# Kernel optimization log

Hardware: AMD Instinct MI355X
Metric: run time of the kernel (lower is better)

Reference implementation:

```python
import jax, jax.numpy as jnp
import numpy as np

N, NFEAT, NHID, NCLASS, NHEADS = 50000, 512, 256, 64, 8
C1 = NHID // NHEADS  # 32 per-head channels, layer 1
NEG_SLOPE = 0.2


def setup_inputs() -> dict:
    key = jax.random.key(0)
    ks = jax.random.split(key, 10)
    x = jax.random.normal(ks[0], (N, NFEAT), dtype=jnp.float32)
    edge_idx = jax.random.randint(ks[1], (2, 800000), 0, N, dtype=jnp.int64)
    s = 0.05
    return {
        "x": x,
        "edge_idx": edge_idx,
        "W1": jax.random.normal(ks[2], (NFEAT, NHEADS, C1), dtype=jnp.float32) * s,
        "a1_src": jax.random.normal(ks[3], (NHEADS, C1), dtype=jnp.float32) * s,
        "a1_dst": jax.random.normal(ks[4], (NHEADS, C1), dtype=jnp.float32) * s,
        "b1": jnp.zeros((NHID,), dtype=jnp.float32),
        "W2": jax.random.normal(ks[5], (NHID, NHEADS, NCLASS), dtype=jnp.float32) * s,
        "a2_src": jax.random.normal(ks[6], (NHEADS, NCLASS), dtype=jnp.float32) * s,
        "a2_dst": jax.random.normal(ks[7], (NHEADS, NCLASS), dtype=jnp.float32) * s,
        "b2": jnp.zeros((NCLASS,), dtype=jnp.float32),
    }


def gat_conv(x, src, dst, W, a_src, a_dst, b, concat):
    # x: [N, F_in]; W: [F_in, H, C]; a_*: [H, C]; src/dst: [E]
    h = jnp.einsum("nf,fhc->nhc", x, W)             # [N, H, C]
    e_src = jnp.sum(h * a_src, axis=-1)              # [N, H]
    e_dst = jnp.sum(h * a_dst, axis=-1)              # [N, H]
    alpha = e_src[src] + e_dst[dst]                  # [E, H]
    alpha = jnp.where(alpha > 0, alpha, NEG_SLOPE * alpha)  # leaky_relu(0.2)
    # segment softmax over incoming edges of each destination node
    m = jax.ops.segment_max(alpha, dst, num_segments=N)     # [N, H]
    m = jnp.where(jnp.isfinite(m), m, 0.0)
    e = jnp.exp(alpha - m[dst])                      # [E, H]
    z = jax.ops.segment_sum(e, dst, num_segments=N)  # [N, H]
    coef = e / z[dst]                                # [E, H]
    msg = h[src] * coef[:, :, None]                  # [E, H, C]
    out = jax.ops.segment_sum(msg, dst, num_segments=N)  # [N, H, C]
    if concat:
        out = out.reshape(N, -1)
    else:
        out = out.mean(axis=1)
    return out + b


def reference(x, edge_idx, W1, a1_src, a1_dst, b1, W2, a2_src, a2_dst, b2):
    # add self loops (PyG GATConv default)
    loop = jnp.arange(N, dtype=edge_idx.dtype)
    src = jnp.concatenate([edge_idx[0], loop])
    dst = jnp.concatenate([edge_idx[1], loop])
    h = gat_conv(x, src, dst, W1, a1_src, a1_dst, b1, concat=True)   # [N, NHID]
    h = jax.nn.relu(h)
    # dropout inactive (eval mode)
    out = gat_conv(h, src, dst, W2, a2_src, a2_dst, b2, concat=False)  # [N, NCLASS]
    return jax.nn.log_softmax(out, axis=1)
```

## Files before the change

kernel.cpp:

```cpp
#include <hip/hip_runtime.h>
#include <math.h>

#define NN 50000
#define NF 512
#define NHID 256
#define NCLASS 64
#define NHEADS 8

typedef __attribute__((ext_vector_type(8))) short bf16x8;
typedef __attribute__((ext_vector_type(4))) float f32x4;
typedef __attribute__((ext_vector_type(2))) float f32x2;
typedef __attribute__((ext_vector_type(4))) unsigned int u32x4;
typedef __attribute__((ext_vector_type(2))) unsigned int u32x2;

static __device__ __forceinline__ unsigned short f2bf(float f) {
  unsigned int u = __float_as_uint(f);
  unsigned int r = (u + 0x7fffu + ((u >> 16) & 1u)) >> 16;
  return (unsigned short)r;
}
static __device__ __forceinline__ float bf2f(unsigned short u) {
  return __uint_as_float(((unsigned int)u) << 16);
}
static __device__ __forceinline__ float2 bfpair(unsigned int u) {
  return make_float2(__uint_as_float(u << 16), __uint_as_float(u & 0xffff0000u));
}

static __device__ __forceinline__ u32x2 gld64(const void* p) {
  u32x2 r;
  asm volatile("global_load_dwordx2 %0, %1, off"
               : "=v"(r) : "v"((unsigned long long)p));
  return r;
}
static __device__ __forceinline__ int gld32i(const void* p) {
  int r;
  asm volatile("global_load_dword %0, %1, off"
               : "=v"(r) : "v"((unsigned long long)p));
  return r;
}
static __device__ __forceinline__ float gld32f(const void* p) {
  float r;
  asm volatile("global_load_dword %0, %1, off"
               : "=v"(r) : "v"((unsigned long long)p));
  return r;
}
#define VMCNT0()                                        \
  do {                                                  \
    asm volatile("s_waitcnt vmcnt(0)" ::: "memory");    \
    __builtin_amdgcn_sched_barrier(0);                  \
  } while (0)

__global__ void k_init_deg(int* deg) {
  int i = blockIdx.x * blockDim.x + threadIdx.x;
  if (i < NN) deg[i] = 1;
}

__global__ void k_count(const int* __restrict__ dst, int E0, int* deg) {
  int i = blockIdx.x * blockDim.x + threadIdx.x;
  if (i < E0) atomicAdd(&deg[dst[i]], 1);
}

__global__ __launch_bounds__(1024) void k_scan(const int* __restrict__ deg, int* offs,
                                               int* cursor) {
  __shared__ int wbase[16];
  __shared__ int srun;
  int tid = threadIdx.x;
  int lane = tid & 63;
  int wv = tid >> 6;
  if (tid == 0) srun = 0;
  __syncthreads();
  for (int base = 0; base < NN; base += 4096) {
    int i = base + tid * 4;
    int4 v;
    if (i + 3 < NN) {
      v = *(const int4*)(deg + i);
    } else {
      v.x = (i + 0 < NN) ? deg[i + 0] : 0;
      v.y = (i + 1 < NN) ? deg[i + 1] : 0;
      v.z = (i + 2 < NN) ? deg[i + 2] : 0;
      v.w = (i + 3 < NN) ? deg[i + 3] : 0;
    }
    int tot = v.x + v.y + v.z + v.w;
    int s = tot;
    #pragma unroll
    for (int o = 1; o < 64; o <<= 1) {
      int t = __shfl_up(s, o);
      if (lane >= o) s += t;
    }
    if (lane == 63) wbase[wv] = s;
    __syncthreads();
    if (tid == 0) {
      int run = srun;
      #pragma unroll
      for (int w2 = 0; w2 < 16; w2++) {
        int t = wbase[w2];
        wbase[w2] = run;
        run += t;
      }
      srun = run;
    }
    __syncthreads();
    int p = wbase[wv] + s - tot;
    if (i + 0 < NN) { offs[i + 0] = p; cursor[i + 0] = p; p += v.x; }
    if (i + 1 < NN) { offs[i + 1] = p; cursor[i + 1] = p; p += v.y; }
    if (i + 2 < NN) { offs[i + 2] = p; cursor[i + 2] = p; p += v.z; }
    if (i + 3 < NN) { offs[i + 3] = p; cursor[i + 3] = p; }
  }
  __syncthreads();
  if (tid == 0) offs[NN] = srun;
}

__global__ void k_scatter(const int* __restrict__ src, const int* __restrict__ dst,
                          int E0, int* cursor, int* __restrict__ nbr) {
  int i = blockIdx.x * blockDim.x + threadIdx.x;
  if (i < E0) {
    int pos = atomicAdd(&cursor[dst[i]], 1);
    nbr[pos] = src[i];
  } else if (i < E0 + NN) {
    int v = i - E0;
    int pos = atomicAdd(&cursor[v], 1);
    nbr[pos] = v;
  }
}

__global__ void k_cast4(const float* __restrict__ in, unsigned short* __restrict__ out,
                        int n4) {
  int i = blockIdx.x * blockDim.x + threadIdx.x;
  if (i >= n4) return;
  float4 v = *(const float4*)(in + (size_t)i * 4);
  ushort4 o;
  o.x = f2bf(v.x); o.y = f2bf(v.y); o.z = f2bf(v.z); o.w = f2bf(v.w);
  *(ushort4*)(out + (size_t)i * 4) = o;
}

__global__ void k_castWt(const float* __restrict__ W, unsigned short* __restrict__ Wt,
                         int K, int cols) {
  int i = blockIdx.x * blockDim.x + threadIdx.x;
  if (i >= K * cols) return;
  int k = i / cols, c = i % cols;
  Wt[(size_t)c * K + k] = f2bf(W[i]);
}

__global__ void k_castWt_perm(const float* __restrict__ W, unsigned short* __restrict__ Wt,
                              int K) {
  int i = blockIdx.x * blockDim.x + threadIdx.x;
  if (i >= K * NHEADS * NCLASS) return;
  int k = i / (NHEADS * NCLASS);
  int rem = i % (NHEADS * NCLASS);
  int h = rem / NCLASS, c = rem % NCLASS;
  Wt[(size_t)(c * NHEADS + h) * K + k] = f2bf(W[i]);
}

__global__ void k_cast_fp8(const unsigned short* __restrict__ in,
                           unsigned char* __restrict__ out, int n8) {
  int i = blockIdx.x * blockDim.x + threadIdx.x;
  if (i >= n8) return;
  uint4 raw = *(const uint4*)(in + (size_t)i * 8);
  float2 p0 = bfpair(raw.x), p1 = bfpair(raw.y), p2 = bfpair(raw.z), p3 = bfpair(raw.w);
  int lo = 0, hi = 0;
  lo = __builtin_amdgcn_cvt_pk_fp8_f32(p0.x, p0.y, lo, false);
  lo = __builtin_amdgcn_cvt_pk_fp8_f32(p1.x, p1.y, lo, true);
  hi = __builtin_amdgcn_cvt_pk_fp8_f32(p2.x, p2.y, hi, false);
  hi = __builtin_amdgcn_cvt_pk_fp8_f32(p3.x, p3.y, hi, true);
  u32x2 o; o[0] = (unsigned int)lo; o[1] = (unsigned int)hi;
  *(u32x2*)(out + (size_t)i * 8) = o;
}

__global__ __launch_bounds__(256) void k_gemm_bf(const unsigned short* __restrict__ A,
                                                 const unsigned short* __restrict__ Bt,
                                                 unsigned short* __restrict__ C,
                                                 int rows, int K, int cols) {
  __shared__ unsigned short Bs[256 * 40];
  int t = threadIdx.x;
  int wave = t >> 6, lane = t & 63;
  int quad = lane >> 4, sixt = lane & 15;
  int rb = blockIdx.x * 64 + (wave >> 1) * 32;
  int cw = (wave & 1) * 128;
  int cbw = blockIdx.y * 256 + cw;
  int r0 = rb + sixt, r1 = rb + 16 + sixt;
  const unsigned short* Ap0 = A + (size_t)(r0 < rows ? r0 : 0) * K + quad * 8;
  const unsigned short* Ap1 = A + (size_t)(r1 < rows ? r1 : 0) * K + quad * 8;
  const unsigned short* Bg = Bt + (size_t)(blockIdx.y * 256 + (t >> 2)) * K + (t & 3) * 8;
  const size_t BgStep = (size_t)64 * K;
  char* BsW = (char*)Bs + (t >> 2) * 80 + (t & 3) * 16;
  f32x4 acc0[8] = {}, acc1[8] = {};
  for (int k0 = 0; k0 < K; k0 += 32) {
    uint4 v0 = *(const uint4*)(Bg + k0);
    uint4 v1 = *(const uint4*)(Bg + BgStep + k0);
    uint4 v2 = *(const uint4*)(Bg + 2 * BgStep + k0);
    uint4 v3 = *(const uint4*)(Bg + 3 * BgStep + k0);
    bf16x8 a0 = *(const bf16x8*)(Ap0 + k0);
    bf16x8 a1 = *(const bf16x8*)(Ap1 + k0);
    *(uint4*)(BsW) = v0;
    *(uint4*)(BsW + 64 * 80) = v1;
    *(uint4*)(BsW + 128 * 80) = v2;
    *(uint4*)(BsW + 192 * 80) = v3;
    __syncthreads();
    #pragma unroll
    for (int g = 0; g < 8; g++) {
      bf16x8 b = *(const bf16x8*)((const char*)Bs + (cw + g * 16 + sixt) * 80 + quad * 16);
      acc0[g] = __builtin_amdgcn_mfma_f32_16x16x32_bf16(a0, b, acc0[g], 0, 0, 0);
      acc1[g] = __builtin_amdgcn_mfma_f32_16x16x32_bf16(a1, b, acc1[g], 0, 0, 0);
    }
    __syncthreads();
  }
  #pragma unroll
  for (int r = 0; r < 4; r++) {
    int row = rb + quad * 4 + r;
    if (row < rows) {
      unsigned short* out = C + (size_t)row * cols + cbw + sixt;
      #pragma unroll
      for (int g = 0; g < 8; g++) out[g * 16] = f2bf(acc0[g][r]);
    }
    int row2 = row + 16;
    if (row2 < rows) {
      unsigned short* out = C + (size_t)row2 * cols + cbw + sixt;
      #pragma unroll
      for (int g = 0; g < 8; g++) out[g * 16] = f2bf(acc1[g][r]);
    }
  }
}

__global__ __launch_bounds__(256) void k_gemm_bf8(const unsigned short* __restrict__ A,
                                                  const unsigned short* __restrict__ Bt,
                                                  unsigned char* __restrict__ C,
                                                  int rows, int K, int cols) {
  __shared__ unsigned short Bs[256 * 40];
  int t = threadIdx.x;
  int wave = t >> 6, lane = t & 63;
  int quad = lane >> 4, sixt = lane & 15;
  int rb = blockIdx.x * 64 + (wave >> 1) * 32;
  int cw = (wave & 1) * 128;
  int cbw = blockIdx.y * 256 + cw;
  int r0 = rb + sixt, r1 = rb + 16 + sixt;
  const unsigned short* Ap0 = A + (size_t)(r0 < rows ? r0 : 0) * K + quad * 8;
  const unsigned short* Ap1 = A + (size_t)(r1 < rows ? r1 : 0) * K + quad * 8;
  const unsigned short* Bg = Bt + (size_t)(blockIdx.y * 256 + (t >> 2)) * K + (t & 3) * 8;
  const size_t BgStep = (size_t)64 * K;
  char* BsW = (char*)Bs + (t >> 2) * 80 + (t & 3) * 16;
  f32x4 acc0[8] = {}, acc1[8] = {};
  for (int k0 = 0; k0 < K; k0 += 32) {
    uint4 v0 = *(const uint4*)(Bg + k0);
    uint4 v1 = *(const uint4*)(Bg + BgStep + k0);
    uint4 v2 = *(const uint4*)(Bg + 2 * BgStep + k0);
    uint4 v3 = *(const uint4*)(Bg + 3 * BgStep + k0);
    bf16x8 a0 = *(const bf16x8*)(Ap0 + k0);
    bf16x8 a1 = *(const bf16x8*)(Ap1 + k0);
    *(uint4*)(BsW) = v0;
    *(uint4*)(BsW + 64 * 80) = v1;
    *(uint4*)(BsW + 128 * 80) = v2;
    *(uint4*)(BsW + 192 * 80) = v3;
    __syncthreads();
    #pragma unroll
    for (int g = 0; g < 8; g++) {
      bf16x8 b = *(const bf16x8*)((const char*)Bs + (cw + g * 16 + sixt) * 80 + quad * 16);
      acc0[g] = __builtin_amdgcn_mfma_f32_16x16x32_bf16(a0, b, acc0[g], 0, 0, 0);
      acc1[g] = __builtin_amdgcn_mfma_f32_16x16x32_bf16(a1, b, acc1[g], 0, 0, 0);
    }
    __syncthreads();
  }
  #pragma unroll
  for (int r = 0; r < 4; r++) {
    int row = rb + quad * 4 + r;
    if (row < rows) {
      unsigned char* out = C + (size_t)row * cols + cbw + sixt;
      #pragma unroll
      for (int g = 0; g < 8; g++) {
        int wq = __builtin_amdgcn_cvt_pk_fp8_f32(acc0[g][r], acc0[g][r], 0, false);
        out[g * 16] = (unsigned char)(wq & 0xff);
      }
    }
    int row2 = row + 16;
    if (row2 < rows) {
      unsigned char* out = C + (size_t)row2 * cols + cbw + sixt;
      #pragma unroll
      for (int g = 0; g < 8; g++) {
        int wq = __builtin_amdgcn_cvt_pk_fp8_f32(acc1[g][r], acc1[g][r], 0, false);
        out[g * 16] = (unsigned char)(wq & 0xff);
      }
    }
  }
}

template <int C>
__global__ void k_escore_c(const unsigned short* __restrict__ h,
                           const float* __restrict__ asr, const float* __restrict__ ads,
                           float* __restrict__ es, float* __restrict__ ed) {
  int idx = blockIdx.x * blockDim.x + threadIdx.x;
  if (idx >= NN * NHEADS) return;
  int hd = idx & 7;
  const unsigned short* row = h + (size_t)idx * C;
  float s = 0.f, d = 0.f;
  #pragma unroll
  for (int c8 = 0; c8 < C / 8; c8++) {
    uint4 raw = *(const uint4*)(row + c8 * 8);
    float2 p0 = bfpair(raw.x), p1 = bfpair(raw.y), p2 = bfpair(raw.z), p3 = bfpair(raw.w);
    const float* as_ = asr + hd * C + c8 * 8;
    const float* ad_ = ads + hd * C + c8 * 8;
    s += p0.x * as_[0] + p0.y * as_[1] + p1.x * as_[2] + p1.y * as_[3] +
         p2.x * as_[4] + p2.y * as_[5] + p3.x * as_[6] + p3.y * as_[7];
    d += p0.x * ad_[0] + p0.y * ad_[1] + p1.x * ad_[2] + p1.y * ad_[3] +
         p2.x * ad_[4] + p2.y * ad_[5] + p3.x * ad_[6] + p3.y * ad_[7];
  }
  es[idx] = s;
  ed[idx] = d;
}

__global__ void k_escore_p8(const unsigned char* __restrict__ h,
                            const float* __restrict__ asr, const float* __restrict__ ads,
                            float* __restrict__ es, float* __restrict__ ed) {
  int idx = blockIdx.x * blockDim.x + threadIdx.x;
  if (idx >= NN * NHEADS) return;
  int hd = idx & 7;
  int n = idx >> 3;
  const unsigned short* rp =
      (const unsigned short*)(h + (size_t)n * (NHEADS * NCLASS) + (hd & ~1));
  int hi = hd & 1;
  float s = 0.f, d = 0.f;
  #pragma unroll
  for (int c = 0; c < NCLASS; c++) {
    unsigned short w = rp[c * 4];
    f32x2 q = __builtin_amdgcn_cvt_pk_f32_fp8((int)w, false);
    float v = hi ? q.y : q.x;
    s += v * asr[hd * NCLASS + c];
    d += v * ads[hd * NCLASS + c];
  }
  es[idx] = s;
  ed[idx] = d;
}

__global__ __launch_bounds__(256) void k_agg1f(const int* __restrict__ offs,
                                               const int* __restrict__ nbr,
                                               const unsigned char* __restrict__ h1f8,
                                               const float* __restrict__ es,
                                               const float* __restrict__ ed,
                                               const float* __restrict__ b1,
                                               unsigned short* __restrict__ out) {
  int node = blockIdx.x * 4 + (threadIdx.x >> 6);
  if (node >= NN) return;
  int lane = threadIdx.x & 63;
  int h = lane & 7;
  int sub = lane >> 3;
  int col = lane << 2;
  int beg = offs[node], end = offs[node + 1];
  float edst = ed[node * NHEADS + h];
  int kb = beg;
  int iA = kb + (lane & 7); if (iA > end - 1) iA = end - 1;
  int vt = gld32i(nbr + iA);
  int vtN = 0;
  if (kb + 8 < end) {
    int iB = kb + 8 + (lane & 7); if (iB > end - 1) iB = end - 1;
    vtN = gld32i(nbr + iB);
  }
  VMCNT0();
  int se[8];
  #pragma unroll
  for (int e = 0; e < 8; e++) se[e] = __shfl(vt, e);
  float esv;
  {
    int sv = __shfl(vt, sub);
    esv = gld32f(es + (size_t)sv * NHEADS + h);
  }
  VMCNT0();
  float m = -1e30f, z = 0.f;
  float4 acc = make_float4(0.f, 0.f, 0.f, 0.f);
  while (true) {
    int cnt = end - kb; if (cnt > 8) cnt = 8;
    int r[8];
    #pragma unroll
    for (int e = 0; e < 8; e++)
      if (e < cnt) r[e] = gld32i(h1f8 + (size_t)se[e] * NHID + col);
    bool more = kb + 8 < end, more2 = kb + 16 < end;
    int vt2 = 0;
    if (more2) {
      int iC = kb + 16 + (lane & 7); if (iC > end - 1) iC = end - 1;
      vt2 = gld32i(nbr + iC);
    }
    float esvN = 0.f;
    if (more) {
      int svN = __shfl(vtN, sub);
      esvN = gld32f(es + (size_t)svN * NHEADS + h);
    }
    float ar = esv + edst;
    ar = (ar > 0.f) ? ar : 0.2f * ar;
    float a = (kb + sub < end) ? ar : -1e30f;
    float gm = a;
    #pragma unroll
    for (int o = 8; o < 64; o <<= 1) gm = fmaxf(gm, __shfl_xor(gm, o));
    float mn = fmaxf(m, gm);
    float ee = __expf(a - mn);
    float zg = ee;
    #pragma unroll
    for (int o = 8; o < 64; o <<= 1) zg += __shfl_xor(zg, o);
    float sc = __expf(m - mn);
    z = z * sc + zg;
    m = mn;
    VMCNT0();
    float sch = __shfl(sc, sub);
    acc.x *= sch; acc.y *= sch; acc.z *= sch; acc.w *= sch;
    #pragma unroll
    for (int e = 0; e < 8; e++) {
      if (e < cnt) {
        float ce = __shfl(ee, e * 8 + sub);
        f32x2 q0 = __builtin_amdgcn_cvt_pk_f32_fp8(r[e], false);
        f32x2 q1 = __builtin_amdgcn_cvt_pk_f32_fp8(r[e], true);
        acc.x += ce * q0.x;
        acc.y += ce * q0.y;
        acc.z += ce * q1.x;
        acc.w += ce * q1.y;
      }
    }
    if (!more) break;
    kb += 8;
    #pragma unroll
    for (int e = 0; e < 8; e++) se[e] = __shfl(vtN, e);
    esv = esvN;
    vtN = vt2;
  }
  float inv = 1.f / z;
  float ivh = __shfl(inv, sub);
  ushort4 o;
  o.x = f2bf(fmaxf(acc.x * ivh + b1[col + 0], 0.f));
  o.y = f2bf(fmaxf(acc.y * ivh + b1[col + 1], 0.f));
  o.z = f2bf(fmaxf(acc.z * ivh + b1[col + 2], 0.f));
  o.w = f2bf(fmaxf(acc.w * ivh + b1[col + 3], 0.f));
  *(ushort4*)(out + (size_t)node * NHID + col) = o;
}

__global__ __launch_bounds__(256) void k_agg2f(const int* __restrict__ offs,
                                               const int* __restrict__ nbr,
                                               const unsigned char* __restrict__ h2f8,
                                               const float* __restrict__ es,
                                               const float* __restrict__ ed,
                                               const float* __restrict__ b2,
                                               float* __restrict__ out) {
  __shared__ __align__(16) float cs[4][64];
  int wv = threadIdx.x >> 6;
  int node = blockIdx.x * 4 + wv;
  if (node >= NN) return;
  int lane = threadIdx.x & 63;
  int h = lane & 7;
  int sub = lane >> 3;
  int beg = offs[node], end = offs[node + 1];
  float edst = ed[node * NHEADS + h];
  int kb = beg;
  int iA = kb + (lane & 7); if (iA > end - 1) iA = end - 1;
  int vt = gld32i(nbr + iA);
  int vtN = 0;
  if (kb + 8 < end) {
    int iB = kb + 8 + (lane & 7); if (iB > end - 1) iB = end - 1;
    vtN = gld32i(nbr + iB);
  }
  VMCNT0();
  int se[8];
  #pragma unroll
  for (int e = 0; e < 8; e++) se[e] = __shfl(vt, e);
  float esv;
  {
    int sv = __shfl(vt, sub);
    esv = gld32f(es + (size_t)sv * NHEADS + h);
  }
  VMCNT0();
  float m = -1e30f, z = 0.f;
  float acc[8] = {};
  while (true) {
    int cnt = end - kb; if (cnt > 8) cnt = 8;
    u32x2 r[8];
    #pragma unroll
    for (int e = 0; e < 8; e++)
      if (e < cnt) r[e] = gld64(h2f8 + (size_t)se[e] * (NHEADS * NCLASS) + (lane << 3));
    bool more = kb + 8 < end, more2 = kb + 16 < end;
    int vt2 = 0;
    if (more2) {
      int iC = kb + 16 + (lane & 7); if (iC > end - 1) iC = end - 1;
      vt2 = gld32i(nbr + iC);
    }
    float esvN = 0.f;
    if (more) {
      int svN = __shfl(vtN, sub);
      esvN = gld32f(es + (size_t)svN * NHEADS + h);
    }
    float ar = esv + edst;
    ar = (ar > 0.f) ? ar : 0.2f * ar;
    float a = (kb + sub < end) ? ar : -1e30f;
    float gm = a;
    #pragma unroll
    for (int o = 8; o < 64; o <<= 1) gm = fmaxf(gm, __shfl_xor(gm, o));
    float mn = fmaxf(m, gm);
    float ee = __expf(a - mn);
    float zg = ee;
    #pragma unroll
    for (int o = 8; o < 64; o <<= 1) zg += __shfl_xor(zg, o);
    float sc = __expf(m - mn);
    z = z * sc + zg;
    m = mn;
    cs[wv][lane] = ee;
    VMCNT0();
    #pragma unroll
    for (int hh = 0; hh < 8; hh++) acc[hh] *= __shfl(sc, hh);
    #pragma unroll
    for (int e = 0; e < 8; e++) {
      if (e < cnt) {
        float4 cA = *(const float4*)&cs[wv][e * 8];
        float4 cB = *(const float4*)&cs[wv][e * 8 + 4];
        f32x2 q0 = __builtin_amdgcn_cvt_pk_f32_fp8((int)r[e][0], false);
        f32x2 q1 = __builtin_amdgcn_cvt_pk_f32_fp8((int)r[e][0], true);
        f32x2 q2 = __builtin_amdgcn_cvt_pk_f32_fp8((int)r[e][1], false);
        f32x2 q3 = __builtin_amdgcn_cvt_pk_f32_fp8((int)r[e][1], true);
        acc[0] += cA.x * q0.x;
        acc[1] += cA.y * q0.y;
        acc[2] += cA.z * q1.x;
        acc[3] += cA.w * q1.y;
        acc[4] += cB.x * q2.x;
        acc[5] += cB.y * q2.y;
        acc[6] += cB.z * q3.x;
        acc[7] += cB.w * q3.y;
      }
    }
    if (!more) break;
    kb += 8;
    #pragma unroll
    for (int e = 0; e < 8; e++) se[e] = __shfl(vtN, e);
    esv = esvN;
    vtN = vt2;
  }
  float inv = 1.f / z;
  float val = 0.f;
  #pragma unroll
  for (int hh = 0; hh < 8; hh++) val += acc[hh] * __shfl(inv, hh);
  val = val * 0.125f + b2[lane];
  float mx = val;
  #pragma unroll
  for (int o = 32; o > 0; o >>= 1) mx = fmaxf(mx, __shfl_xor(mx, o));
  float ex = __expf(val - mx);
  float sm = ex;
  #pragma unroll
  for (int o = 32; o > 0; o >>= 1) sm += __shfl_xor(sm, o);
  out[(size_t)node * NCLASS + lane] = val - mx - __logf(sm);
}

extern "C" void kernel_launch(void* const* d_in, const int* in_sizes, int n_in,
                              void* d_out, int out_size, void* d_ws, size_t ws_size,
                              hipStream_t stream) {
  const float* x   = (const float*)d_in[0];
  const int* eidx  = (const int*)d_in[1];
  const float* W1  = (const float*)d_in[2];
  const float* a1s = (const float*)d_in[3];
  const float* a1d = (const float*)d_in[4];
  const float* b1  = (const float*)d_in[5];
  const float* W2  = (const float*)d_in[6];
  const float* a2s = (const float*)d_in[7];
  const float* a2d = (const float*)d_in[8];
  const float* b2  = (const float*)d_in[9];
  const int E0 = in_sizes[1] / 2;
  const int* esrc = eidx;
  const int* edst = eidx + E0;
  const int E = E0 + NN;

  char* w = (char*)d_ws;
  auto carve = [&](size_t bytes) {
    void* p = (void*)w;
    w += (bytes + 255) & ~(size_t)255;
    return p;
  };
  int* deg      = (int*)carve((size_t)NN * 4);
  int* offs     = (int*)carve((size_t)(NN + 1) * 4);
  int* cursor   = (int*)carve((size_t)NN * 4);
  int* nbr      = (int*)carve((size_t)E * 4);
  float* es1    = (float*)carve((size_t)NN * NHEADS * 4);
  float* ed1    = (float*)carve((size_t)NN * NHEADS * 4);
  unsigned short* xbf   = (unsigned short*)carve((size_t)NN * NF * 2);
  unsigned short* W1t   = (unsigned short*)carve((size_t)NF * NHID * 2);
  unsigned short* W2t   = (unsigned short*)carve((size_t)NHID * NHEADS * NCLASS * 2);
  unsigned short* h1b   = (unsigned short*)carve((size_t)NN * NHID * 2);
  unsigned short* out1b = (unsigned short*)carve((size_t)NN * NHID * 2);
  unsigned char* h1f8   = (unsigned char*)carve((size_t)NN * NHID);
  unsigned char* h2f8 = (unsigned char*)xbf;

  k_init_deg<<<(NN + 255) / 256, 256, 0, stream>>>(deg);
  k_count<<<(E0 + 255) / 256, 256, 0, stream>>>(edst, E0, deg);
  k_scan<<<1, 1024, 0, stream>>>(deg, offs, cursor);
  k_scatter<<<(E0 + NN + 255) / 256, 256, 0, stream>>>(esrc, edst, E0, cursor, nbr);

  k_cast4<<<(NN * NF / 4 + 255) / 256, 256, 0, stream>>>(x, xbf, NN * NF / 4);
  k_castWt<<<(NF * NHID + 255) / 256, 256, 0, stream>>>(W1, W1t, NF, NHID);
  k_castWt_perm<<<(NHID * NHEADS * NCLASS + 255) / 256, 256, 0, stream>>>(W2, W2t, NHID);

  k_gemm_bf<<<dim3((NN + 63) / 64, NHID / 256), 256, 0, stream>>>(xbf, W1t, h1b,
                                                                  NN, NF, NHID);
  k_escore_c<32><<<(NN * NHEADS + 255) / 256, 256, 0, stream>>>(h1b, a1s, a1d, es1, ed1);
  k_cast_fp8<<<(NN * NHID / 8 + 255) / 256, 256, 0, stream>>>(h1b, h1f8, NN * NHID / 8);
  k_agg1f<<<(NN + 3) / 4, 256, 0, stream>>>(offs, nbr, h1f8, es1, ed1, b1, out1b);

  k_gemm_bf8<<<dim3((NN + 63) / 64, (NHEADS * NCLASS) / 256), 256, 0, stream>>>(
      out1b, W2t, h2f8, NN, NHID, NHEADS * NCLASS);
  k_escore_p8<<<(NN * NHEADS + 255) / 256, 256, 0, stream>>>(h2f8, a2s, a2d, es1, ed1);
  k_agg2f<<<(NN + 3) / 4, 256, 0, stream>>>(offs, nbr, h2f8, es1, ed1, b2,
                                            (float*)d_out);
}
```

Baseline: 548.0 us.

## Parallelize degree scan, fuse fp8 cast into GEMM, widen aggregation batches to 16 edges

New measurement: 540.4 us. Within noise of the previous version (-1.4%).

```diff
diff --git a/kernel.cpp b/kernel.cpp
--- a/kernel.cpp
+++ b/kernel.cpp
@@ -6,11 +6,11 @@
 #define NHID 256
 #define NCLASS 64
 #define NHEADS 8
+#define SCAN_NBLK ((NN + 1023) / 1024)
 
 typedef __attribute__((ext_vector_type(8))) short bf16x8;
 typedef __attribute__((ext_vector_type(4))) float f32x4;
 typedef __attribute__((ext_vector_type(2))) float f32x2;
-typedef __attribute__((ext_vector_type(4))) unsigned int u32x4;
 typedef __attribute__((ext_vector_type(2))) unsigned int u32x2;
 
 static __device__ __forceinline__ unsigned short f2bf(float f) {
@@ -59,54 +59,68 @@
   if (i < E0) atomicAdd(&deg[dst[i]], 1);
 }
 
-__global__ __launch_bounds__(1024) void k_scan(const int* __restrict__ deg, int* offs,
-                                               int* cursor) {
-  __shared__ int wbase[16];
-  __shared__ int srun;
+__global__ __launch_bounds__(256) void k_scanA(const int* __restrict__ deg, int* offs,
+                                               int* bsum) {
+  __shared__ int wsum[4];
   int tid = threadIdx.x;
   int lane = tid & 63;
   int wv = tid >> 6;
-  if (tid == 0) srun = 0;
+  int i = blockIdx.x * 1024 + tid * 4;
+  int4 v = make_int4(0, 0, 0, 0);
+  if (i + 3 < NN) {
+    v = *(const int4*)(deg + i);
+  } else {
+    if (i + 0 < NN) v.x = deg[i + 0];
+    if (i + 1 < NN) v.y = deg[i + 1];
+    if (i + 2 < NN) v.z = deg[i + 2];
+    if (i + 3 < NN) v.w = deg[i + 3];
+  }
+  int tot = v.x + v.y + v.z + v.w;
+  int s = tot;
+  #pragma unroll
+  for (int o = 1; o < 64; o <<= 1) {
+    int t = __shfl_up(s, o);
+    if (lane >= o) s += t;
+  }
+  if (lane == 63) wsum[wv] = s;
   __syncthreads();
-  for (int base = 0; base < NN; base += 4096) {
-    int i = base + tid * 4;
-    int4 v;
-    if (i + 3 < NN) {
-      v = *(const int4*)(deg + i);
-    } else {
-      v.x = (i + 0 < NN) ? deg[i + 0] : 0;
-      v.y = (i + 1 < NN) ? deg[i + 1] : 0;
-      v.z = (i + 2 < NN) ? deg[i + 2] : 0;
-      v.w = (i + 3 < NN) ? deg[i + 3] : 0;
-    }
-    int tot = v.x + v.y + v.z + v.w;
-    int s = tot;
-    #pragma unroll
-    for (int o = 1; o < 64; o <<= 1) {
-      int t = __shfl_up(s, o);
-      if (lane >= o) s += t;
-    }
-    if (lane == 63) wbase[wv] = s;
-    __syncthreads();
-    if (tid == 0) {
-      int run = srun;
-      #pragma unroll
-      for (int w2 = 0; w2 < 16; w2++) {
-        int t = wbase[w2];
-        wbase[w2] = run;
-        run += t;
-      }
-      srun = run;
-    }
-    __syncthreads();
-    int p = wbase[wv] + s - tot;
-    if (i + 0 < NN) { offs[i + 0] = p; cursor[i + 0] = p; p += v.x; }
-    if (i + 1 < NN) { offs[i + 1] = p; cursor[i + 1] = p; p += v.y; }
-    if (i + 2 < NN) { offs[i + 2] = p; cursor[i + 2] = p; p += v.z; }
-    if (i + 3 < NN) { offs[i + 3] = p; cursor[i + 3] = p; }
-  }
-  __syncthreads();
-  if (tid == 0) offs[NN] = srun;
+  int base = 0;
+  #pragma unroll
+  for (int w2 = 0; w2 < 4; w2++)
+    if (w2 < wv) base += wsum[w2];
+  int p = base + s - tot;
+  if (i + 0 < NN) { offs[i + 0] = p; p += v.x; }
+  if (i + 1 < NN) { offs[i + 1] = p; p += v.y; }
+  if (i + 2 < NN) { offs[i + 2] = p; p += v.z; }
+  if (i + 3 < NN) { offs[i + 3] = p; }
+  if (tid == 255) bsum[blockIdx.x] = base + s;
+}
+
+__global__ void k_scanB(const int* __restrict__ bsum, int* bbase, int* offs, int nb) {
+  int lane = threadIdx.x;
+  int v = (lane < nb) ? bsum[lane] : 0;
+  int s = v;
+  #pragma unroll
+  for (int o = 1; o < 64; o <<= 1) {
+    int t = __shfl_up(s, o);
+    if (lane >= o) s += t;
+  }
+  if (lane < nb) bbase[lane] = s - v;
+  if (lane == 63) offs[NN] = s;
+}
+
+__global__ __launch_bounds__(256) void k_scanC(int* offs, int* cursor,
+                                               const int* __restrict__ bbase) {
+  int add = bbase[blockIdx.x];
+  int i = blockIdx.x * 1024 + threadIdx.x * 4;
+  #pragma unroll
+  for (int j = 0; j < 4; j++) {
+    if (i + j < NN) {
+      int o = offs[i + j] + add;
+      offs[i + j] = o;
+      cursor[i + j] = o;
+    }
+  }
 }
 
 __global__ void k_scatter(const int* __restrict__ src, const int* __restrict__ dst,
@@ -150,25 +164,11 @@
   Wt[(size_t)(c * NHEADS + h) * K + k] = f2bf(W[i]);
 }
 
-__global__ void k_cast_fp8(const unsigned short* __restrict__ in,
-                           unsigned char* __restrict__ out, int n8) {
-  int i = blockIdx.x * blockDim.x + threadIdx.x;
-  if (i >= n8) return;
-  uint4 raw = *(const uint4*)(in + (size_t)i * 8);
-  float2 p0 = bfpair(raw.x), p1 = bfpair(raw.y), p2 = bfpair(raw.z), p3 = bfpair(raw.w);
-  int lo = 0, hi = 0;
-  lo = __builtin_amdgcn_cvt_pk_fp8_f32(p0.x, p0.y, lo, false);
-  lo = __builtin_amdgcn_cvt_pk_fp8_f32(p1.x, p1.y, lo, true);
-  hi = __builtin_amdgcn_cvt_pk_fp8_f32(p2.x, p2.y, hi, false);
-  hi = __builtin_amdgcn_cvt_pk_fp8_f32(p3.x, p3.y, hi, true);
-  u32x2 o; o[0] = (unsigned int)lo; o[1] = (unsigned int)hi;
-  *(u32x2*)(out + (size_t)i * 8) = o;
-}
-
-__global__ __launch_bounds__(256) void k_gemm_bf(const unsigned short* __restrict__ A,
-                                                 const unsigned short* __restrict__ Bt,
-                                                 unsigned short* __restrict__ C,
-                                                 int rows, int K, int cols) {
+__global__ __launch_bounds__(256) void k_gemm_bf_dual(const unsigned short* __restrict__ A,
+                                                      const unsigned short* __restrict__ Bt,
+                                                      unsigned short* __restrict__ C,
+                                                      unsigned char* __restrict__ C8,
+                                                      int rows, int K, int cols) {
   __shared__ unsigned short Bs[256 * 40];
   int t = threadIdx.x;
   int wave = t >> 6, lane = t & 63;
@@ -208,14 +208,24 @@
     int row = rb + quad * 4 + r;
     if (row < rows) {
       unsigned short* out = C + (size_t)row * cols + cbw + sixt;
+      unsigned char* out8 = C8 + (size_t)row * cols + cbw + sixt;
       #pragma unroll
-      for (int g = 0; g < 8; g++) out[g * 16] = f2bf(acc0[g][r]);
+      for (int g = 0; g < 8; g++) {
+        out[g * 16] = f2bf(acc0[g][r]);
+        int wq = __builtin_amdgcn_cvt_pk_fp8_f32(acc0[g][r], acc0[g][r], 0, false);
+        out8[g * 16] = (unsigned char)(wq & 0xff);
+      }
     }
     int row2 = row + 16;
     if (row2 < rows) {
       unsigned short* out = C + (size_t)row2 * cols + cbw + sixt;
+      unsigned char* out8 = C8 + (size_t)row2 * cols + cbw + sixt;
       #pragma unroll
-      for (int g = 0; g < 8; g++) out[g * 16] = f2bf(acc1[g][r]);
+      for (int g = 0; g < 8; g++) {
+        out[g * 16] = f2bf(acc1[g][r]);
+        int wq = __builtin_amdgcn_cvt_pk_fp8_f32(acc1[g][r], acc1[g][r], 0, false);
+        out8[g * 16] = (unsigned char)(wq & 0xff);
+      }
     }
   }
 }
@@ -344,51 +354,59 @@
   int beg = offs[node], end = offs[node + 1];
   float edst = ed[node * NHEADS + h];
   int kb = beg;
-  int iA = kb + (lane & 7); if (iA > end - 1) iA = end - 1;
-  int vt = gld32i(nbr + iA);
+  int i0 = kb + (lane & 15); if (i0 > end - 1) i0 = end - 1;
+  int vt = gld32i(nbr + i0);
   int vtN = 0;
-  if (kb + 8 < end) {
-    int iB = kb + 8 + (lane & 7); if (iB > end - 1) iB = end - 1;
-    vtN = gld32i(nbr + iB);
+  if (kb + 16 < end) {
+    int i1 = kb + 16 + (lane & 15); if (i1 > end - 1) i1 = end - 1;
+    vtN = gld32i(nbr + i1);
   }
   VMCNT0();
-  int se[8];
-  #pragma unroll
-  for (int e = 0; e < 8; e++) se[e] = __shfl(vt, e);
-  float esv;
+  int se[16];
+  #pragma unroll
+  for (int e = 0; e < 16; e++) se[e] = __shfl(vt, e);
+  float esv0, esv1;
   {
-    int sv = __shfl(vt, sub);
-    esv = gld32f(es + (size_t)sv * NHEADS + h);
+    int sv0 = __shfl(vt, sub);
+    int sv1 = __shfl(vt, sub + 8);
+    esv0 = gld32f(es + (size_t)sv0 * NHEADS + h);
+    esv1 = gld32f(es + (size_t)sv1 * NHEADS + h);
   }
   VMCNT0();
   float m = -1e30f, z = 0.f;
   float4 acc = make_float4(0.f, 0.f, 0.f, 0.f);
   while (true) {
-    int cnt = end - kb; if (cnt > 8) cnt = 8;
-    int r[8];
-    #pragma unroll
-    for (int e = 0; e < 8; e++)
+    int cnt = end - kb; if (cnt > 16) cnt = 16;
+    int r[16];
+    #pragma unroll
+    for (int e = 0; e < 16; e++)
       if (e < cnt) r[e] = gld32i(h1f8 + (size_t)se[e] * NHID + col);
-    bool more = kb + 8 < end, more2 = kb + 16 < end;
+    bool more = kb + 16 < end, more2 = kb + 32 < end;
     int vt2 = 0;
     if (more2) {
-      int iC = kb + 16 + (lane & 7); if (iC > end - 1) iC = end - 1;
+      int iC = kb + 32 + (lane & 15); if (iC > end - 1) iC = end - 1;
       vt2 = gld32i(nbr + iC);
     }
-    float esvN = 0.f;
+    float esvN0 = 0.f, esvN1 = 0.f;
     if (more) {
-      int svN = __shfl(vtN, sub);
-      esvN = gld32f(es + (size_t)svN * NHEADS + h);
-    }
-    float ar = esv + edst;
-    ar = (ar > 0.f) ? ar : 0.2f * ar;
-    float a = (kb + sub < end) ? ar : -1e30f;
-    float gm = a;
+      int sv0 = __shfl(vtN, sub);
+      int sv1 = __shfl(vtN, sub + 8);
+      esvN0 = gld32f(es + (size_t)sv0 * NHEADS + h);
+      esvN1 = gld32f(es + (size_t)sv1 * NHEADS + h);
+    }
+    float ar0 = esv0 + edst;
+    ar0 = (ar0 > 0.f) ? ar0 : 0.2f * ar0;
+    float a0 = (kb + sub < end) ? ar0 : -1e30f;
+    float ar1 = esv1 + edst;
+    ar1 = (ar1 > 0.f) ? ar1 : 0.2f * ar1;
+    float a1 = (kb + sub + 8 < end) ? ar1 : -1e30f;
+    float gm = fmaxf(a0, a1);
     #pragma unroll
     for (int o = 8; o < 64; o <<= 1) gm = fmaxf(gm, __shfl_xor(gm, o));
     float mn = fmaxf(m, gm);
-    float ee = __expf(a - mn);
-    float zg = ee;
+    float ee0 = __expf(a0 - mn);
+    float ee1 = __expf(a1 - mn);
+    float zg = ee0 + ee1;
     #pragma unroll
     for (int o = 8; o < 64; o <<= 1) zg += __shfl_xor(zg, o);
     float sc = __expf(m - mn);
@@ -398,9 +416,9 @@
     float sch = __shfl(sc, sub);
     acc.x *= sch; acc.y *= sch; acc.z *= sch; acc.w *= sch;
     #pragma unroll
-    for (int e = 0; e < 8; e++) {
+    for (int e = 0; e < 16; e++) {
       if (e < cnt) {
-        float ce = __shfl(ee, e * 8 + sub);
+        float ce = (e < 8) ? __shfl(ee0, e * 8 + sub) : __shfl(ee1, (e - 8) * 8 + sub);
         f32x2 q0 = __builtin_amdgcn_cvt_pk_f32_fp8(r[e], false);
         f32x2 q1 = __builtin_amdgcn_cvt_pk_f32_fp8(r[e], true);
         acc.x += ce * q0.x;
@@ -410,10 +428,11 @@
       }
     }
     if (!more) break;
-    kb += 8;
-    #pragma unroll
-    for (int e = 0; e < 8; e++) se[e] = __shfl(vtN, e);
-    esv = esvN;
+    kb += 16;
+    #pragma unroll
+    for (int e = 0; e < 16; e++) se[e] = __shfl(vtN, e);
+    esv0 = esvN0;
+    esv1 = esvN1;
     vtN = vt2;
   }
   float inv = 1.f / z;
@@ -433,7 +452,7 @@
                                                const float* __restrict__ ed,
                                                const float* __restrict__ b2,
                                                float* __restrict__ out) {
-  __shared__ __align__(16) float cs[4][64];
+  __shared__ __align__(16) float cs[4][128];
   int wv = threadIdx.x >> 6;
   int node = blockIdx.x * 4 + wv;
   if (node >= NN) return;
@@ -443,62 +462,71 @@
   int beg = offs[node], end = offs[node + 1];
   float edst = ed[node * NHEADS + h];
   int kb = beg;
-  int iA = kb + (lane & 7); if (iA > end - 1) iA = end - 1;
-  int vt = gld32i(nbr + iA);
+  int i0 = kb + (lane & 15); if (i0 > end - 1) i0 = end - 1;
+  int vt = gld32i(nbr + i0);
   int vtN = 0;
-  if (kb + 8 < end) {
-    int iB = kb + 8 + (lane & 7); if (iB > end - 1) iB = end - 1;
-    vtN = gld32i(nbr + iB);
+  if (kb + 16 < end) {
+    int i1 = kb + 16 + (lane & 15); if (i1 > end - 1) i1 = end - 1;
+    vtN = gld32i(nbr + i1);
   }
   VMCNT0();
-  int se[8];
-  #pragma unroll
-  for (int e = 0; e < 8; e++) se[e] = __shfl(vt, e);
-  float esv;
+  int se[16];
+  #pragma unroll
+  for (int e = 0; e < 16; e++) se[e] = __shfl(vt, e);
+  float esv0, esv1;
   {
-    int sv = __shfl(vt, sub);
-    esv = gld32f(es + (size_t)sv * NHEADS + h);
+    int sv0 = __shfl(vt, sub);
+    int sv1 = __shfl(vt, sub + 8);
+    esv0 = gld32f(es + (size_t)sv0 * NHEADS + h);
+    esv1 = gld32f(es + (size_t)sv1 * NHEADS + h);
   }
   VMCNT0();
   float m = -1e30f, z = 0.f;
   float acc[8] = {};
   while (true) {
-    int cnt = end - kb; if (cnt > 8) cnt = 8;
-    u32x2 r[8];
-    #pragma unroll
-    for (int e = 0; e < 8; e++)
+    int cnt = end - kb; if (cnt > 16) cnt = 16;
+    u32x2 r[16];
+    #pragma unroll
+    for (int e = 0; e < 16; e++)
       if (e < cnt) r[e] = gld64(h2f8 + (size_t)se[e] * (NHEADS * NCLASS) + (lane << 3));
-    bool more = kb + 8 < end, more2 = kb + 16 < end;
+    bool more = kb + 16 < end, more2 = kb + 32 < end;
     int vt2 = 0;
     if (more2) {
-      int iC = kb + 16 + (lane & 7); if (iC > end - 1) iC = end - 1;
+      int iC = kb + 32 + (lane & 15); if (iC > end - 1) iC = end - 1;
       vt2 = gld32i(nbr + iC);
     }
-    float esvN = 0.f;
+    float esvN0 = 0.f, esvN1 = 0.f;
     if (more) {
-      int svN = __shfl(vtN, sub);
-      esvN = gld32f(es + (size_t)svN * NHEADS + h);
-    }
-    float ar = esv + edst;
-    ar = (ar > 0.f) ? ar : 0.2f * ar;
-    float a = (kb + sub < end) ? ar : -1e30f;
-    float gm = a;
+      int sv0 = __shfl(vtN, sub);
+      int sv1 = __shfl(vtN, sub + 8);
+      esvN0 = gld32f(es + (size_t)sv0 * NHEADS + h);
+      esvN1 = gld32f(es + (size_t)sv1 * NHEADS + h);
+    }
+    float ar0 = esv0 + edst;
+    ar0 = (ar0 > 0.f) ? ar0 : 0.2f * ar0;
+    float a0 = (kb + sub < end) ? ar0 : -1e30f;
+    float ar1 = esv1 + edst;
+    ar1 = (ar1 > 0.f) ? ar1 : 0.2f * ar1;
+    float a1 = (kb + sub + 8 < end) ? ar1 : -1e30f;
+    float gm = fmaxf(a0, a1);
     #pragma unroll
     for (int o = 8; o < 64; o <<= 1) gm = fmaxf(gm, __shfl_xor(gm, o));
     float mn = fmaxf(m, gm);
-    float ee = __expf(a - mn);
-    float zg = ee;
+    float ee0 = __expf(a0 - mn);
+    float ee1 = __expf(a1 - mn);
+    float zg = ee0 + ee1;
     #pragma unroll
     for (int o = 8; o < 64; o <<= 1) zg += __shfl_xor(zg, o);
     float sc = __expf(m - mn);
     z = z * sc + zg;
     m = mn;
-    cs[wv][lane] = ee;
+    cs[wv][lane] = ee0;
+    cs[wv][64 + lane] = ee1;
     VMCNT0();
     #pragma unroll
     for (int hh = 0; hh < 8; hh++) acc[hh] *= __shfl(sc, hh);
     #pragma unroll
-    for (int e = 0; e < 8; e++) {
+    for (int e = 0; e < 16; e++) {
       if (e < cnt) {
         float4 cA = *(const float4*)&cs[wv][e * 8];
         float4 cB = *(const float4*)&cs[wv][e * 8 + 4];
@@ -517,10 +545,11 @@
       }
     }
     if (!more) break;
-    kb += 8;
-    #pragma unroll
-    for (int e = 0; e < 8; e++) se[e] = __shfl(vtN, e);
-    esv = esvN;
+    kb += 16;
+    #pragma unroll
+    for (int e = 0; e < 16; e++) se[e] = __shfl(vtN, e);
+    esv0 = esvN0;
+    esv1 = esvN1;
     vtN = vt2;
   }
   float inv = 1.f / z;
@@ -566,6 +595,8 @@
   int* offs     = (int*)carve((size_t)(NN + 1) * 4);
   int* cursor   = (int*)carve((size_t)NN * 4);
   int* nbr      = (int*)carve((size_t)E * 4);
+  int* bsum     = (int*)carve((size_t)64 * 4);
+  int* bbase    = (int*)carve((size_t)64 * 4);
   float* es1    = (float*)carve((size_t)NN * NHEADS * 4);
   float* ed1    = (float*)carve((size_t)NN * NHEADS * 4);
   unsigned short* xbf   = (unsigned short*)carve((size_t)NN * NF * 2);
@@ -578,17 +609,18 @@
 
   k_init_deg<<<(NN + 255) / 256, 256, 0, stream>>>(deg);
   k_count<<<(E0 + 255) / 256, 256, 0, stream>>>(edst, E0, deg);
-  k_scan<<<1, 1024, 0, stream>>>(deg, offs, cursor);
+  k_scanA<<<SCAN_NBLK, 256, 0, stream>>>(deg, offs, bsum);
+  k_scanB<<<1, 64, 0, stream>>>(bsum, bbase, offs, SCAN_NBLK);
+  k_scanC<<<SCAN_NBLK, 256, 0, stream>>>(offs, cursor, bbase);
   k_scatter<<<(E0 + NN + 255) / 256, 256, 0, stream>>>(esrc, edst, E0, cursor, nbr);
 
   k_cast4<<<(NN * NF / 4 + 255) / 256, 256, 0, stream>>>(x, xbf, NN * NF / 4);
   k_castWt<<<(NF * NHID + 255) / 256, 256, 0, stream>>>(W1, W1t, NF, NHID);
   k_castWt_perm<<<(NHID * NHEADS * NCLASS + 255) / 256, 256, 0, stream>>>(W2, W2t, NHID);
 
-  k_gemm_bf<<<dim3((NN + 63) / 64, NHID / 256), 256, 0, stream>>>(xbf, W1t, h1b,
-                                                                  NN, NF, NHID);
+  k_gemm_bf_dual<<<dim3((NN + 63) / 64, NHID / 256), 256, 0, stream>>>(
+      xbf, W1t, h1b, h1f8, NN, NF, NHID);
   k_escore_c<32><<<(NN * NHEADS + 255) / 256, 256, 0, stream>>>(h1b, a1s, a1d, es1, ed1);
-  k_cast_fp8<<<(NN * NHID / 8 + 255) / 256, 256, 0, stream>>>(h1b, h1f8, NN * NHID / 8);
   k_agg1f<<<(NN + 3) / 4, 256, 0, stream>>>(offs, nbr, h1f8, es1, ed1, b1, out1b);
 
   k_gemm_bf8<<<dim3((NN + 63) / 64, (NHEADS * NCLASS) / 256), 256, 0, stream>>>(
```
